# Optimization experiments

Measured on AMD Instinct MI355X. Metric: run time of the kernel, lower is better.

## Reference

```python
import jax, jax.numpy as jnp
import numpy as np

V, E, T_MAX, H, L = 20000, 384, 512, 8, 8
D = E // H  # head size 48
FF = 4 * E


def setup_inputs() -> dict:
    key = jax.random.key(0)
    ks = jax.random.split(key, 24)
    B, T = 16, 512
    s = 0.02
    return {
        "index": jax.random.randint(ks[0], (B, T), 0, V, dtype=jnp.int64),
        "targets": jax.random.randint(ks[1], (B, T), 0, V, dtype=jnp.int64),
        "tok_emb": s * jax.random.normal(ks[2], (V, E), jnp.float32),
        "pos_emb": s * jax.random.normal(ks[3], (T_MAX, E), jnp.float32),
        "Wq": s * jax.random.normal(ks[4], (L, E, H, D), jnp.float32),
        "bq": jnp.zeros((L, H, D), jnp.float32),
        "Wk": s * jax.random.normal(ks[5], (L, E, H, D), jnp.float32),
        "bk": jnp.zeros((L, H, D), jnp.float32),
        "Wv": s * jax.random.normal(ks[6], (L, E, H, D), jnp.float32),
        "bv": jnp.zeros((L, H, D), jnp.float32),
        "Wo": s * jax.random.normal(ks[7], (L, E, E), jnp.float32),
        "bo": jnp.zeros((L, E), jnp.float32),
        "ln1_g": jnp.ones((L, E), jnp.float32),
        "ln1_b": jnp.zeros((L, E), jnp.float32),
        "ln2_g": jnp.ones((L, E), jnp.float32),
        "ln2_b": jnp.zeros((L, E), jnp.float32),
        "W1": s * jax.random.normal(ks[8], (L, E, FF), jnp.float32),
        "b1": jnp.zeros((L, FF), jnp.float32),
        "W2": s * jax.random.normal(ks[9], (L, FF, E), jnp.float32),
        "b2": jnp.zeros((L, E), jnp.float32),
        "lnf_g": jnp.ones((E,), jnp.float32),
        "lnf_b": jnp.zeros((E,), jnp.float32),
        "lm_b": jnp.zeros((V,), jnp.float32),
    }


def layernorm(x, g, b, eps=1e-5):
    mu = jnp.mean(x, axis=-1, keepdims=True)
    var = jnp.var(x, axis=-1, keepdims=True)
    return (x - mu) * jax.lax.rsqrt(var + eps) * g + b


def reference(index, targets, tok_emb, pos_emb, Wq, bq, Wk, bk, Wv, bv, Wo, bo,
              ln1_g, ln1_b, ln2_g, ln2_b, W1, b1, W2, b2, lnf_g, lnf_b, lm_b):
    B, T = index.shape
    x = tok_emb[index] + pos_emb[:T]  # [B,T,E]
    causal = jnp.tril(jnp.ones((T, T), bool))
    scale = D ** -0.5
    for l in range(L):
        h = layernorm(x, ln1_g[l], ln1_b[l])
        q = jnp.einsum('bte,ehd->bthd', h, Wq[l]) + bq[l]
        k = jnp.einsum('bte,ehd->bthd', h, Wk[l]) + bk[l]
        v = jnp.einsum('bte,ehd->bthd', h, Wv[l]) + bv[l]
        scores = jnp.einsum('bqhd,bkhd->bhqk', q, k) * scale
        scores = jnp.where(causal, scores, -jnp.inf)
        w = jax.nn.softmax(scores, axis=-1)
        attn = jnp.einsum('bhqk,bkhd->bqhd', w, v).reshape(B, T, E)
        x = x + attn @ Wo[l] + bo[l]
        h2 = layernorm(x, ln2_g[l], ln2_b[l])
        ff = jax.nn.gelu(h2 @ W1[l] + b1[l], approximate=False) @ W2[l] + b2[l]
        x = x + ff
    x = layernorm(x, lnf_g, lnf_b)
    logits = x @ tok_emb.T + lm_b  # tied weights
    logits = logits.reshape(B * T, V)
    logp = jax.nn.log_softmax(logits, axis=-1)
    loss = -jnp.mean(jnp.take_along_axis(logp, targets.reshape(-1, 1), axis=-1))
    return logits, loss
```

## Files before the change

kernel.cpp:

```cpp
#include <hip/hip_runtime.h>
#include <hip/hip_bf16.h>
#include <math.h>

#define M_ROWS 8192
#define E_DIM 384
#define FF_DIM 1536
#define V_DIM 20000
#define VPAD 20096
#define N_LAYER 8
#define QK_SCALE 0.14433756729740643f
#define PSTRIDE 320
#define NPART 314

typedef __bf16 bf16x8 __attribute__((ext_vector_type(8)));
typedef short  s16x8  __attribute__((ext_vector_type(8)));
typedef float  f32x4  __attribute__((ext_vector_type(4)));
typedef __hip_bfloat16 bf16_t;

__device__ __forceinline__ void gl2lds16(const void* g, void* l) {
    __builtin_amdgcn_global_load_lds((const __attribute__((address_space(1))) void*)g,
                                     (__attribute__((address_space(3))) void*)l, 16, 0, 0);
}
__device__ __forceinline__ unsigned short bf16bits(float v) {
    return __builtin_bit_cast(unsigned short, __float2bfloat16(v));
}

__global__ __launch_bounds__(256) void tconv_kernel(
    const float* __restrict__ in, bf16_t* __restrict__ out,
    int K, int N, int outRows, int rowoff)
{
    __shared__ float tile[32][33];
    const int n0 = blockIdx.x * 32, k0 = blockIdx.y * 32;
    const float* ip = in + (size_t)blockIdx.z * K * N;
    bf16_t* op = out + (size_t)blockIdx.z * outRows * K;
    const int tx = threadIdx.x & 31, ty = threadIdx.x >> 5;
#pragma unroll
    for (int i = 0; i < 32; i += 8)
        tile[ty + i][tx] = ip[(size_t)(k0 + ty + i) * N + n0 + tx];
    __syncthreads();
#pragma unroll
    for (int i = 0; i < 32; i += 8)
        op[(size_t)(rowoff + n0 + ty + i) * K + k0 + tx] = __float2bfloat16(tile[tx][ty + i]);
}

__global__ __launch_bounds__(256) void tokconv_kernel(
    const float* __restrict__ tok, bf16_t* __restrict__ out)
{
    const size_t total = (size_t)VPAD * E_DIM;
    for (size_t i = blockIdx.x * 256ull + threadIdx.x; i < total; i += gridDim.x * 256ull) {
        int row = (int)(i / E_DIM);
        int col = (int)(i - (size_t)row * E_DIM);
        float v = (row < V_DIM) ? tok[(size_t)row * E_DIM + col] : 0.f;
        out[i] = __float2bfloat16(v);
    }
}

__global__ __launch_bounds__(256) void bqkv_kernel(
    const float* __restrict__ bq, const float* __restrict__ bk,
    const float* __restrict__ bv, float* __restrict__ o)
{
    int i = blockIdx.x * 256 + threadIdx.x;
    if (i < N_LAYER * 1152) {
        int l = i / 1152, c = i - l * 1152;
        float v = (c < 384) ? bq[l * 384 + c] : (c < 768) ? bk[l * 384 + c - 384] : bv[l * 384 + c - 768];
        o[i] = v;
    }
}

__global__ __launch_bounds__(256) void embed_kernel(
    const int* __restrict__ idx, const float* __restrict__ tok,
    const float* __restrict__ pos, float* __restrict__ x)
{
    int row = blockIdx.x * 4 + (threadIdx.x >> 6);
    int lane = threadIdx.x & 63;
    int t = row & 511;
    int id = idx[row];
    const float* tr = tok + (size_t)id * E_DIM;
    const float* pr = pos + (size_t)t * E_DIM;
    float* xr = x + (size_t)row * E_DIM;
#pragma unroll
    for (int i = 0; i < 6; i++) { int c = lane + i * 64; xr[c] = tr[c] + pr[c]; }
}

__global__ __launch_bounds__(256) void ln_kernel(
    const float* __restrict__ x, const float* __restrict__ g,
    const float* __restrict__ b, bf16_t* __restrict__ out)
{
    int row = blockIdx.x * 4 + (threadIdx.x >> 6);
    int lane = threadIdx.x & 63;
    const float* xr = x + (size_t)row * E_DIM;
    float vals[6];
    float s = 0.f;
#pragma unroll
    for (int i = 0; i < 6; i++) { vals[i] = xr[lane + i * 64]; s += vals[i]; }
#pragma unroll
    for (int off = 1; off < 64; off <<= 1) s += __shfl_xor(s, off);
    float mu = s * (1.f / E_DIM);
    float sq = 0.f;
#pragma unroll
    for (int i = 0; i < 6; i++) { float d = vals[i] - mu; sq += d * d; }
#pragma unroll
    for (int off = 1; off < 64; off <<= 1) sq += __shfl_xor(sq, off);
    float rstd = rsqrtf(sq * (1.f / E_DIM) + 1e-5f);
    bf16_t* orow = out + (size_t)row * E_DIM;
#pragma unroll
    for (int i = 0; i < 6; i++) {
        int c = lane + i * 64;
        orow[c] = __float2bfloat16((vals[i] - mu) * rstd * g[c] + b[c]);
    }
}

template <int MODE, int MREP, bool SWAP>
__global__ __launch_bounds__(256) void gemm_kernel(
    const bf16_t* __restrict__ A, const bf16_t* __restrict__ Bt,
    const float* __restrict__ bias, void* __restrict__ Cv, void* __restrict__ C2,
    int Ncols, int K)
{
    constexpr int BMR = MREP * 32;
    constexpr int BUFSH = BMR * 32 + 4096;
    __shared__ __align__(16) short smem[2 * BUFSH];
    const int t = threadIdx.x;
    const int w = t >> 6, lane = t & 63;
    const int wm = w >> 1, wn = w & 1;
    const int bm = (MODE == 3 ? blockIdx.x : blockIdx.y) * BMR;
    const int bn = (MODE == 3 ? blockIdx.y : blockIdx.x) * 128;

    f32x4 acc[MREP][4];
#pragma unroll
    for (int m = 0; m < MREP; m++)
#pragma unroll
        for (int n = 0; n < 4; n++)
            acc[m][n] = (f32x4){0.f, 0.f, 0.f, 0.f};

    const int lg = lane >> 4;
    const int ll = lane & 15;
    const int nt = K / 32;

    auto stagef = [&](int kt, int buf) {
        short* sA = smem + buf * BUFSH;
        short* sB = sA + BMR * 32;
#pragma unroll
        for (int i = 0; i < MREP / 2; i++) {
            int li = i * 256 + t;
            int g = li >> (MREP == 4 ? 7 : 6);
            int row = li & (BMR - 1);
            gl2lds16(A + (size_t)(bm + row) * K + kt + g * 8,
                     sA + (size_t)(i * 256 + w * 64) * 8);
        }
#pragma unroll
        for (int i = 0; i < 2; i++) {
            int li = i * 256 + t;
            gl2lds16(Bt + (size_t)(bn + (li & 127)) * K + kt + (li >> 7) * 8,
                     sB + (size_t)(i * 256 + w * 64) * 8);
        }
    };

    stagef(0, 0);
    asm volatile("s_waitcnt vmcnt(0)" ::: "memory");
    __builtin_amdgcn_s_barrier();

    for (int tt = 0; tt < nt; ++tt) {
        const int cur = tt & 1;
        if (tt + 1 < nt) stagef((tt + 1) * 32, cur ^ 1);

        const short* sA = smem + cur * BUFSH;
        const short* sB = sA + BMR * 32;
        bf16x8 af[MREP], bfr[4];
#pragma unroll
        for (int m = 0; m < MREP; m++)
            af[m] = __builtin_bit_cast(bf16x8,
                *(const s16x8*)&sA[(lg * BMR + wm * (BMR / 2) + m * 16 + ll) * 8]);
#pragma unroll
        for (int n = 0; n < 4; n++)
            bfr[n] = __builtin_bit_cast(bf16x8,
                *(const s16x8*)&sB[(lg * 128 + wn * 64 + n * 16 + ll) * 8]);
#pragma unroll
        for (int m = 0; m < MREP; m++)
#pragma unroll
            for (int n = 0; n < 4; n++) {
                if (SWAP)
                    acc[m][n] = __builtin_amdgcn_mfma_f32_16x16x32_bf16(bfr[n], af[m], acc[m][n], 0, 0, 0);
                else
                    acc[m][n] = __builtin_amdgcn_mfma_f32_16x16x32_bf16(af[m], bfr[n], acc[m][n], 0, 0, 0);
            }

        asm volatile("s_waitcnt vmcnt(0)" ::: "memory");
        __builtin_amdgcn_s_barrier();
    }

    if constexpr (SWAP) {
        const int rowm0 = bm + wm * (BMR / 2) + ll;
        const int coln0 = bn + wn * 64 + lg * 4;

        if constexpr (MODE == 4) {
            bf16_t* qkvb = (bf16_t*)Cv;
            const float sc = (bn >= 384) ? 1.f : QK_SCALE;
#pragma unroll
            for (int n = 0; n < 4; n++) {
                const int coln = coln0 + n * 16;
                const float4 b4 = *(const float4*)&bias[coln];
#pragma unroll
                for (int m = 0; m < MREP; m++) {
                    const int row = rowm0 + m * 16;
                    ushort4 pk;
                    pk.x = bf16bits((acc[m][n][0] + b4.x) * sc);
                    pk.y = bf16bits((acc[m][n][1] + b4.y) * sc);
                    pk.z = bf16bits((acc[m][n][2] + b4.z) * sc);
                    pk.w = bf16bits((acc[m][n][3] + b4.w) * sc);
                    *(ushort4*)&qkvb[(size_t)row * 1152 + coln] = pk;
                }
            }
        } else if constexpr (MODE == 1) {
            float* C = (float*)Cv;
#pragma unroll
            for (int n = 0; n < 4; n++) {
                const int coln = coln0 + n * 16;
                const float4 b4 = *(const float4*)&bias[coln];
#pragma unroll
                for (int m = 0; m < MREP; m++) {
                    const int row = rowm0 + m * 16;
                    float4 cv = *(float4*)&C[(size_t)row * Ncols + coln];
                    cv.x += acc[m][n][0] + b4.x;
                    cv.y += acc[m][n][1] + b4.y;
                    cv.z += acc[m][n][2] + b4.z;
                    cv.w += acc[m][n][3] + b4.w;
                    *(float4*)&C[(size_t)row * Ncols + coln] = cv;
                }
            }
        } else if constexpr (MODE == 2) {
            bf16_t* O = (bf16_t*)Cv;
#pragma unroll
            for (int n = 0; n < 4; n++) {
                const int coln = coln0 + n * 16;
                const float4 b4 = *(const float4*)&bias[coln];
#pragma unroll
                for (int m = 0; m < MREP; m++) {
                    const int row = rowm0 + m * 16;
                    float v0 = acc[m][n][0] + b4.x, v1 = acc[m][n][1] + b4.y;
                    float v2 = acc[m][n][2] + b4.z, v3 = acc[m][n][3] + b4.w;
                    v0 = 0.5f * v0 * (1.f + erff(v0 * 0.70710678118654752f));
                    v1 = 0.5f * v1 * (1.f + erff(v1 * 0.70710678118654752f));
                    v2 = 0.5f * v2 * (1.f + erff(v2 * 0.70710678118654752f));
                    v3 = 0.5f * v3 * (1.f + erff(v3 * 0.70710678118654752f));
                    ushort4 pk;
                    pk.x = bf16bits(v0); pk.y = bf16bits(v1);
                    pk.z = bf16bits(v2); pk.w = bf16bits(v3);
                    *(ushort4*)&O[(size_t)row * Ncols + coln] = pk;
                }
            }
        } else if constexpr (MODE == 3) {
            float* C = (float*)Cv;
            float* pbuf = (float*)C2;
            const int ptile = blockIdx.y * 2 + wn;
#pragma unroll
            for (int m = 0; m < MREP; m++) {
                const int row = rowm0 + m * 16;
                float se = 0.f;
#pragma unroll
                for (int n = 0; n < 4; n++) {
                    const int coln = coln0 + n * 16;
                    if (coln + 3 < Ncols) {
                        const float4 b4 = *(const float4*)&bias[coln];
                        float4 v;
                        v.x = acc[m][n][0] + b4.x;
                        v.y = acc[m][n][1] + b4.y;
                        v.z = acc[m][n][2] + b4.z;
                        v.w = acc[m][n][3] + b4.w;
                        *(float4*)&C[(size_t)row * Ncols + coln] = v;
                        se += __expf(v.x) + __expf(v.y) + __expf(v.z) + __expf(v.w);
                    } else {
#pragma unroll
                        for (int e = 0; e < 4; e++) {
                            int col = coln + e;
                            if (col < Ncols) {
                                float v = acc[m][n][e] + bias[col];
                                C[(size_t)row * Ncols + col] = v;
                                se += __expf(v);
                            }
                        }
                    }
                }
                se += __shfl_xor(se, 16);
                se += __shfl_xor(se, 32);
                if (lg == 0) pbuf[(size_t)row * PSTRIDE + ptile] = se;
            }
        }
        return;
    }

    {
        const int r0 = bm + wm * (BMR / 2) + lg * 4;
        const int c0 = bn + wn * 64 + ll;
        bf16_t* vtb = (bf16_t*)C2;
#pragma unroll
        for (int n = 0; n < 4; n++) {
            const int col = c0 + n * 16;
            const float bv = bias[col];
            const int hh = col / 48, dd = col - hh * 48;
#pragma unroll
            for (int m = 0; m < MREP; m++) {
                const int row0 = r0 + m * 16;
                const int bb = row0 >> 9, tt2 = row0 & 511;
                ushort4 pk;
                pk.x = bf16bits(acc[m][n][0] + bv);
                pk.y = bf16bits(acc[m][n][1] + bv);
                pk.z = bf16bits(acc[m][n][2] + bv);
                pk.w = bf16bits(acc[m][n][3] + bv);
                *(ushort4*)&vtb[((size_t)(bb * 8 + hh) * 48 + dd) * 512 + tt2] = pk;
            }
        }
    }
}

__global__ __launch_bounds__(256) void attn_kernel(
    const bf16_t* __restrict__ qkvb, const bf16_t* __restrict__ vt,
    bf16_t* __restrict__ o)
{
    const int qt = blockIdx.x, bh = blockIdx.y;
    const int b = bh >> 3, h = bh & 7;
    __shared__ unsigned short psm[4608];
    const int tid = threadIdx.x;
    const int w = tid >> 6, lane = tid & 63;
    const int ll = lane & 15, g = lane >> 4;
    const int q0 = qt * 64;
    const int q_abs = q0 + ll * 4 + w;

    const bf16_t* qrow = qkvb + (size_t)(b * 512 + q_abs) * 1152 + h * 48;
    bf16x8 qf0 = __builtin_bit_cast(bf16x8, *(const s16x8*)(qrow + g * 8));
    bf16x8 qf1 = {};
    if (g < 2) qf1 = __builtin_bit_cast(bf16x8, *(const s16x8*)(qrow + 32 + g * 8));

    f32x4 oacc[3];
#pragma unroll
    for (int df = 0; df < 3; df++) oacc[df] = (f32x4){0.f, 0.f, 0.f, 0.f};
    float mrun = -1e30f, ssum = 0.f;

    const bf16_t* kptr = qkvb + (size_t)b * 512 * 1152 + 384 + h * 48;
    const bf16_t* vptr = vt + (size_t)bh * 48 * 512;
    const int ntiles = 2 * (qt + 1);

    auto loadK = [&](int kbase, bf16x8& c00, bf16x8& c01, bf16x8& c10, bf16x8& c11) {
        const bf16_t* kr0 = kptr + (size_t)(kbase + ll) * 1152;
        const bf16_t* kr1 = kptr + (size_t)(kbase + 16 + ll) * 1152;
        c00 = __builtin_bit_cast(bf16x8, *(const s16x8*)(kr0 + g * 8));
        c10 = __builtin_bit_cast(bf16x8, *(const s16x8*)(kr1 + g * 8));
        bf16x8 z = {};
        c01 = (g < 2) ? __builtin_bit_cast(bf16x8, *(const s16x8*)(kr0 + 32 + g * 8)) : z;
        c11 = (g < 2) ? __builtin_bit_cast(bf16x8, *(const s16x8*)(kr1 + 32 + g * 8)) : z;
    };

    auto doTile = [&](int kbase, int parity,
                      const bf16x8& c00, const bf16x8& c01, const bf16x8& c10, const bf16x8& c11,
                      bool pf, int nbase,
                      bf16x8& n00, bf16x8& n01, bf16x8& n10, bf16x8& n11) {
        bf16x8 vf[3];
#pragma unroll
        for (int df = 0; df < 3; df++)
            vf[df] = __builtin_bit_cast(bf16x8,
                *(const s16x8*)(vptr + (size_t)(df * 16 + ll) * 512 + kbase + g * 8));
        if (pf) loadK(nbase, n00, n01, n10, n11);

        f32x4 sfr[2];
        {
            f32x4 z0 = {0.f, 0.f, 0.f, 0.f};
            z0 = __builtin_amdgcn_mfma_f32_16x16x32_bf16(c00, qf0, z0, 0, 0, 0);
            z0 = __builtin_amdgcn_mfma_f32_16x16x32_bf16(c01, qf1, z0, 0, 0, 0);
            sfr[0] = z0;
            f32x4 z1 = {0.f, 0.f, 0.f, 0.f};
            z1 = __builtin_amdgcn_mfma_f32_16x16x32_bf16(c10, qf0, z1, 0, 0, 0);
            z1 = __builtin_amdgcn_mfma_f32_16x16x32_bf16(c11, qf1, z1, 0, 0, 0);
            sfr[1] = z1;
        }

        float p[8];
        float tmax = -1e30f;
#pragma unroll
        for (int f = 0; f < 2; f++)
#pragma unroll
            for (int j = 0; j < 4; j++) {
                int key = kbase + f * 16 + g * 4 + j;
                float sv = sfr[f][j];
                sv = (key > q_abs) ? -1e30f : sv;
                p[f * 4 + j] = sv;
                tmax = fmaxf(tmax, sv);
            }
        tmax = fmaxf(tmax, __shfl_xor(tmax, 16));
        tmax = fmaxf(tmax, __shfl_xor(tmax, 32));
        float mnew = fmaxf(mrun, tmax);
        float corr = __expf(mrun - mnew);
        float psum = 0.f;
#pragma unroll
        for (int i = 0; i < 8; i++) { p[i] = __expf(p[i] - mnew); psum += p[i]; }
        psum += __shfl_xor(psum, 16);
        psum += __shfl_xor(psum, 32);
        ssum = ssum * corr + psum;
        mrun = mnew;
#pragma unroll
        for (int df = 0; df < 3; df++)
#pragma unroll
            for (int j = 0; j < 4; j++) oacc[df][j] *= corr;

        const int pbase = (w * 2 + parity) * 576;
#pragma unroll
        for (int f = 0; f < 2; f++)
#pragma unroll
            for (int j = 0; j < 4; j++)
                psm[pbase + (f * 16 + g * 4 + j) * 18 + ll] = bf16bits(p[f * 4 + j]);
        s16x8 pr;
#pragma unroll
        for (int i = 0; i < 8; i++)
            pr[i] = (short)psm[pbase + (g * 8 + i) * 18 + ll];
        bf16x8 pfr = __builtin_bit_cast(bf16x8, pr);
#pragma unroll
        for (int df = 0; df < 3; df++)
            oacc[df] = __builtin_amdgcn_mfma_f32_16x16x32_bf16(vf[df], pfr, oacc[df], 0, 0, 0);
    };

    bf16x8 kA0, kA1, kA2, kA3, kB0, kB1, kB2, kB3;
    loadK(0, kA0, kA1, kA2, kA3);
    for (int kt = 0; kt < ntiles; kt += 2) {
        doTile(kt * 32, 0, kA0, kA1, kA2, kA3,
               true, (kt + 1) * 32, kB0, kB1, kB2, kB3);
        doTile((kt + 1) * 32, 1, kB0, kB1, kB2, kB3,
               (kt + 2) < ntiles, (kt + 2) * 32, kA0, kA1, kA2, kA3);
    }

    float inv = 1.f / ssum;
    bf16_t* orow = o + (size_t)(b * 512 + q_abs) * 384 + h * 48;
#pragma unroll
    for (int df = 0; df < 3; df++) {
        ushort4 pk;
        pk.x = bf16bits(oacc[df][0] * inv);
        pk.y = bf16bits(oacc[df][1] * inv);
        pk.z = bf16bits(oacc[df][2] * inv);
        pk.w = bf16bits(oacc[df][3] * inv);
        *(ushort4*)&orow[df * 16 + g * 4] = pk;
    }
}

__global__ __launch_bounds__(256) void loss_row2_kernel(
    const float* __restrict__ pbuf, const float* __restrict__ logits,
    const int* __restrict__ targets, float* __restrict__ rowloss)
{
    int row = blockIdx.x * 4 + (threadIdx.x >> 6);
    int lane = threadIdx.x & 63;
    const float* pr = pbuf + (size_t)row * PSTRIDE;
    float s = 0.f;
    for (int i = lane; i < NPART; i += 64) s += pr[i];
#pragma unroll
    for (int off = 1; off < 64; off <<= 1) s += __shfl_xor(s, off);
    if (lane == 0) {
        int tgt = targets[row];
        rowloss[row] = logf(s) - logits[(size_t)row * V_DIM + tgt];
    }
}

__global__ __launch_bounds__(256) void loss_reduce_kernel(
    const float* __restrict__ rowloss, float* __restrict__ out)
{
    int t = threadIdx.x;
    __shared__ float red[4];
    float s = 0.f;
    for (int i = t; i < M_ROWS; i += 256) s += rowloss[i];
#pragma unroll
    for (int off = 1; off < 64; off <<= 1) s += __shfl_xor(s, off);
    if ((t & 63) == 0) red[t >> 6] = s;
    __syncthreads();
    if (t == 0) out[0] = (red[0] + red[1] + red[2] + red[3]) * (1.f / M_ROWS);
}

extern "C" void kernel_launch(void* const* d_in, const int* in_sizes, int n_in,
                              void* d_out, int out_size, void* d_ws, size_t ws_size,
                              hipStream_t stream)
{
    const int*   index   = (const int*)d_in[0];
    const int*   targets = (const int*)d_in[1];
    const float* tok_emb = (const float*)d_in[2];
    const float* pos_emb = (const float*)d_in[3];
    const float* Wq = (const float*)d_in[4];
    const float* bq = (const float*)d_in[5];
    const float* Wk = (const float*)d_in[6];
    const float* bk = (const float*)d_in[7];
    const float* Wv = (const float*)d_in[8];
    const float* bv = (const float*)d_in[9];
    const float* Wo = (const float*)d_in[10];
    const float* bo = (const float*)d_in[11];
    const float* ln1_g = (const float*)d_in[12];
    const float* ln1_b = (const float*)d_in[13];
    const float* ln2_g = (const float*)d_in[14];
    const float* ln2_b = (const float*)d_in[15];
    const float* W1 = (const float*)d_in[16];
    const float* b1 = (const float*)d_in[17];
    const float* W2 = (const float*)d_in[18];
    const float* b2 = (const float*)d_in[19];
    const float* lnf_g = (const float*)d_in[20];
    const float* lnf_b = (const float*)d_in[21];
    const float* lm_b  = (const float*)d_in[22];

    float* out = (float*)d_out;
    char* wsb = (char*)d_ws;

    float*  x     = (float*)(wsb + 0);
    bf16_t* hbuf  = (bf16_t*)(wsb + 12582912);
    bf16_t* obuf  = (bf16_t*)(wsb + 18874368);
    bf16_t* qkvb  = (bf16_t*)(wsb + 25165824);
    bf16_t* vtb   = (bf16_t*)(wsb + 44040192);
    bf16_t* ffmid = (bf16_t*)(wsb + 18874368);
    float*  pbuf  = (float*)(wsb + 25165824);
    bf16_t* tokb  = (bf16_t*)(wsb + 50331648);
    bf16_t* qkvw  = (bf16_t*)(wsb + 65765376);
    bf16_t* wo_t  = (bf16_t*)(wsb + 72843264);
    bf16_t* w1_t  = (bf16_t*)(wsb + 75202560);
    bf16_t* w2_t  = (bf16_t*)(wsb + 84639744);
    float*  bqkv  = (float*)(wsb + 94076928);
    float*  rowloss = (float*)(wsb + 94113792);

    tokconv_kernel<<<2048, 256, 0, stream>>>(tok_emb, tokb);
    tconv_kernel<<<dim3(12, 12, 8), 256, 0, stream>>>(Wq, qkvw, 384, 384, 1152, 0);
    tconv_kernel<<<dim3(12, 12, 8), 256, 0, stream>>>(Wk, qkvw, 384, 384, 1152, 384);
    tconv_kernel<<<dim3(12, 12, 8), 256, 0, stream>>>(Wv, qkvw, 384, 384, 1152, 768);
    tconv_kernel<<<dim3(12, 12, 8), 256, 0, stream>>>(Wo, wo_t, 384, 384, 384, 0);
    tconv_kernel<<<dim3(48, 12, 8), 256, 0, stream>>>(W1, w1_t, 384, 1536, 1536, 0);
    tconv_kernel<<<dim3(12, 48, 8), 256, 0, stream>>>(W2, w2_t, 1536, 384, 384, 0);
    bqkv_kernel<<<36, 256, 0, stream>>>(bq, bk, bv, bqkv);

    embed_kernel<<<2048, 256, 0, stream>>>(index, tok_emb, pos_emb, x);

    for (int l = 0; l < N_LAYER; l++) {
        const bf16_t* qkvw_l = qkvw + (size_t)l * 1152 * 384;
        const float*  bqkv_l = bqkv + l * 1152;
        ln_kernel<<<2048, 256, 0, stream>>>(x, ln1_g + l * E_DIM, ln1_b + l * E_DIM, hbuf);
        gemm_kernel<4, 4, true><<<dim3(6, 64), 256, 0, stream>>>(
            hbuf, qkvw_l, bqkv_l, qkvb, nullptr, 1152, 384);
        gemm_kernel<5, 4, false><<<dim3(3, 64), 256, 0, stream>>>(
            hbuf, qkvw_l + (size_t)768 * 384, bqkv_l + 768, nullptr, vtb, 384, 384);
        attn_kernel<<<dim3(8, 128), 256, 0, stream>>>(qkvb, vtb, obuf);
        gemm_kernel<1, 2, true><<<dim3(3, 128), 256, 0, stream>>>(
            obuf, wo_t + (size_t)l * 384 * 384, bo + l * E_DIM, x, nullptr, 384, 384);
        ln_kernel<<<2048, 256, 0, stream>>>(x, ln2_g + l * E_DIM, ln2_b + l * E_DIM, hbuf);
        gemm_kernel<2, 4, true><<<dim3(12, 64), 256, 0, stream>>>(
            hbuf, w1_t + (size_t)l * 1536 * 384, b1 + l * FF_DIM, ffmid, nullptr, 1536, 384);
        gemm_kernel<1, 2, true><<<dim3(3, 128), 256, 0, stream>>>(
            ffmid, w2_t + (size_t)l * 384 * 1536, b2 + l * E_DIM, x, nullptr, 384, 1536);
    }

    ln_kernel<<<2048, 256, 0, stream>>>(x, lnf_g, lnf_b, hbuf);
    gemm_kernel<3, 4, true><<<dim3(64, 157), 256, 0, stream>>>(
        hbuf, tokb, lm_b, out, pbuf, V_DIM, 384);

    loss_row2_kernel<<<2048, 256, 0, stream>>>(pbuf, out, targets, rowloss);
    loss_reduce_kernel<<<1, 256, 0, stream>>>(rowloss, out + (size_t)M_ROWS * V_DIM);
}
```

Baseline: 1.968 ms.

## Triple-buffer GEMM staging, fuse V projection into QKV GEMM, nontemporal logits stores

The GEMM main loop moves from double to triple buffering. Loads are issued two K-tiles ahead, with partial vmcnt waits taken before the barrier instead of draining all loads after the MFMAs. The separate V-transposed GEMM launch is folded into the QKV GEMM: blocks whose columns fall in the V range write a transposed layout with scalar strided stores, and the attention kernel's V pointer is adjusted to match. The LM-head logits and partial sums are written with nontemporal stores to limit cache pollution. In exchange, the kernel needs more LDS, which may lower occupancy, and the scalar transposed V stores are uncoalesced.

```diff
diff --git a/kernel.cpp b/kernel.cpp
--- a/kernel.cpp
+++ b/kernel.cpp
@@ -110,15 +110,17 @@
     }
 }
 
-template <int MODE, int MREP, bool SWAP>
+template <int MODE, int MREP>
 __global__ __launch_bounds__(256) void gemm_kernel(
     const bf16_t* __restrict__ A, const bf16_t* __restrict__ Bt,
     const float* __restrict__ bias, void* __restrict__ Cv, void* __restrict__ C2,
     int Ncols, int K)
 {
     constexpr int BMR = MREP * 32;
-    constexpr int BUFSH = BMR * 32 + 4096;
-    __shared__ __align__(16) short smem[2 * BUFSH];
+    constexpr int ASH = BMR * 32;
+    constexpr int BUFSH = ASH + 4096;
+    constexpr int NLD = MREP / 2 + 2;
+    __shared__ __align__(16) short smem[3 * BUFSH];
     const int t = threadIdx.x;
     const int w = t >> 6, lane = t & 63;
     const int wm = w >> 1, wn = w & 1;
@@ -138,7 +140,7 @@
 
     auto stagef = [&](int kt, int buf) {
         short* sA = smem + buf * BUFSH;
-        short* sB = sA + BMR * 32;
+        short* sB = sA + ASH;
 #pragma unroll
         for (int i = 0; i < MREP / 2; i++) {
             int li = i * 256 + t;
@@ -156,15 +158,21 @@
     };
 
     stagef(0, 0);
-    asm volatile("s_waitcnt vmcnt(0)" ::: "memory");
-    __builtin_amdgcn_s_barrier();
+    stagef(32, 1);
 
     for (int tt = 0; tt < nt; ++tt) {
-        const int cur = tt & 1;
-        if (tt + 1 < nt) stagef((tt + 1) * 32, cur ^ 1);
-
-        const short* sA = smem + cur * BUFSH;
-        const short* sB = sA + BMR * 32;
+        if (tt + 2 < nt) {
+            stagef((tt + 2) * 32, (tt + 2) % 3);
+            asm volatile("s_waitcnt vmcnt(%0)" :: "n"(2 * NLD) : "memory");
+        } else if (tt + 1 < nt) {
+            asm volatile("s_waitcnt vmcnt(%0)" :: "n"(NLD) : "memory");
+        } else {
+            asm volatile("s_waitcnt vmcnt(0)" ::: "memory");
+        }
+        __builtin_amdgcn_s_barrier();
+
+        const short* sA = smem + (tt % 3) * BUFSH;
+        const short* sB = sA + ASH;
         bf16x8 af[MREP], bfr[4];
 #pragma unroll
         for (int m = 0; m < MREP; m++)
@@ -177,22 +185,17 @@
 #pragma unroll
         for (int m = 0; m < MREP; m++)
 #pragma unroll
-            for (int n = 0; n < 4; n++) {
-                if (SWAP)
-                    acc[m][n] = __builtin_amdgcn_mfma_f32_16x16x32_bf16(bfr[n], af[m], acc[m][n], 0, 0, 0);
-                else
-                    acc[m][n] = __builtin_amdgcn_mfma_f32_16x16x32_bf16(af[m], bfr[n], acc[m][n], 0, 0, 0);
-            }
-
-        asm volatile("s_waitcnt vmcnt(0)" ::: "memory");
+            for (int n = 0; n < 4; n++)
+                acc[m][n] = __builtin_amdgcn_mfma_f32_16x16x32_bf16(bfr[n], af[m], acc[m][n], 0, 0, 0);
+
         __builtin_amdgcn_s_barrier();
     }
 
-    if constexpr (SWAP) {
-        const int rowm0 = bm + wm * (BMR / 2) + ll;
-        const int coln0 = bn + wn * 64 + lg * 4;
-
-        if constexpr (MODE == 4) {
+    const int rowm0 = bm + wm * (BMR / 2) + ll;
+    const int coln0 = bn + wn * 64 + lg * 4;
+
+    if constexpr (MODE == 4) {
+        if (bn < 768) {
             bf16_t* qkvb = (bf16_t*)Cv;
             const float sc = (bn >= 384) ? 1.f : QK_SCALE;
 #pragma unroll
@@ -210,104 +213,98 @@
                     *(ushort4*)&qkvb[(size_t)row * 1152 + coln] = pk;
                 }
             }
-        } else if constexpr (MODE == 1) {
-            float* C = (float*)Cv;
+        } else {
+            bf16_t* vtb = (bf16_t*)C2;
+            const int cc0 = coln0 - 768;
+#pragma unroll
+            for (int n = 0; n < 4; n++) {
+                const float4 b4 = *(const float4*)&bias[coln0 + n * 16];
+#pragma unroll
+                for (int m = 0; m < MREP; m++) {
+                    const int row = rowm0 + m * 16;
+                    const int bb = row >> 9, tt2 = row & 511;
+                    bf16_t* vb = vtb + (size_t)bb * 384 * 512 + tt2;
+                    vb[(size_t)(cc0 + n * 16 + 0) * 512] = __float2bfloat16(acc[m][n][0] + b4.x);
+                    vb[(size_t)(cc0 + n * 16 + 1) * 512] = __float2bfloat16(acc[m][n][1] + b4.y);
+                    vb[(size_t)(cc0 + n * 16 + 2) * 512] = __float2bfloat16(acc[m][n][2] + b4.z);
+                    vb[(size_t)(cc0 + n * 16 + 3) * 512] = __float2bfloat16(acc[m][n][3] + b4.w);
+                }
+            }
+        }
+    } else if constexpr (MODE == 1) {
+        float* C = (float*)Cv;
+#pragma unroll
+        for (int n = 0; n < 4; n++) {
+            const int coln = coln0 + n * 16;
+            const float4 b4 = *(const float4*)&bias[coln];
+#pragma unroll
+            for (int m = 0; m < MREP; m++) {
+                const int row = rowm0 + m * 16;
+                float4 cv = *(float4*)&C[(size_t)row * Ncols + coln];
+                cv.x += acc[m][n][0] + b4.x;
+                cv.y += acc[m][n][1] + b4.y;
+                cv.z += acc[m][n][2] + b4.z;
+                cv.w += acc[m][n][3] + b4.w;
+                *(float4*)&C[(size_t)row * Ncols + coln] = cv;
+            }
+        }
+    } else if constexpr (MODE == 2) {
+        bf16_t* O = (bf16_t*)Cv;
+#pragma unroll
+        for (int n = 0; n < 4; n++) {
+            const int coln = coln0 + n * 16;
+            const float4 b4 = *(const float4*)&bias[coln];
+#pragma unroll
+            for (int m = 0; m < MREP; m++) {
+                const int row = rowm0 + m * 16;
+                float v0 = acc[m][n][0] + b4.x, v1 = acc[m][n][1] + b4.y;
+                float v2 = acc[m][n][2] + b4.z, v3 = acc[m][n][3] + b4.w;
+                v0 = 0.5f * v0 * (1.f + erff(v0 * 0.70710678118654752f));
+                v1 = 0.5f * v1 * (1.f + erff(v1 * 0.70710678118654752f));
+                v2 = 0.5f * v2 * (1.f + erff(v2 * 0.70710678118654752f));
+                v3 = 0.5f * v3 * (1.f + erff(v3 * 0.70710678118654752f));
+                ushort4 pk;
+                pk.x = bf16bits(v0); pk.y = bf16bits(v1);
+                pk.z = bf16bits(v2); pk.w = bf16bits(v3);
+                *(ushort4*)&O[(size_t)row * Ncols + coln] = pk;
+            }
+        }
+    } else if constexpr (MODE == 3) {
+        float* C = (float*)Cv;
+        float* pbuf = (float*)C2;
+        const int ptile = blockIdx.y * 2 + wn;
+#pragma unroll
+        for (int m = 0; m < MREP; m++) {
+            const int row = rowm0 + m * 16;
+            float se = 0.f;
 #pragma unroll
             for (int n = 0; n < 4; n++) {
                 const int coln = coln0 + n * 16;
-                const float4 b4 = *(const float4*)&bias[coln];
-#pragma unroll
-                for (int m = 0; m < MREP; m++) {
-                    const int row = rowm0 + m * 16;
-                    float4 cv = *(float4*)&C[(size_t)row * Ncols + coln];
-                    cv.x += acc[m][n][0] + b4.x;
-                    cv.y += acc[m][n][1] + b4.y;
-                    cv.z += acc[m][n][2] + b4.z;
-                    cv.w += acc[m][n][3] + b4.w;
-                    *(float4*)&C[(size_t)row * Ncols + coln] = cv;
-                }
-            }
-        } else if constexpr (MODE == 2) {
-            bf16_t* O = (bf16_t*)Cv;
-#pragma unroll
-            for (int n = 0; n < 4; n++) {
-                const int coln = coln0 + n * 16;
-                const float4 b4 = *(const float4*)&bias[coln];
-#pragma unroll
-                for (int m = 0; m < MREP; m++) {
-                    const int row = rowm0 + m * 16;
-                    float v0 = acc[m][n][0] + b4.x, v1 = acc[m][n][1] + b4.y;
-                    float v2 = acc[m][n][2] + b4.z, v3 = acc[m][n][3] + b4.w;
-                    v0 = 0.5f * v0 * (1.f + erff(v0 * 0.70710678118654752f));
-                    v1 = 0.5f * v1 * (1.f + erff(v1 * 0.70710678118654752f));
-                    v2 = 0.5f * v2 * (1.f + erff(v2 * 0.70710678118654752f));
-                    v3 = 0.5f * v3 * (1.f + erff(v3 * 0.70710678118654752f));
-                    ushort4 pk;
-                    pk.x = bf16bits(v0); pk.y = bf16bits(v1);
-                    pk.z = bf16bits(v2); pk.w = bf16bits(v3);
-                    *(ushort4*)&O[(size_t)row * Ncols + coln] = pk;
-                }
-            }
-        } else if constexpr (MODE == 3) {
-            float* C = (float*)Cv;
-            float* pbuf = (float*)C2;
-            const int ptile = blockIdx.y * 2 + wn;
-#pragma unroll
-            for (int m = 0; m < MREP; m++) {
-                const int row = rowm0 + m * 16;
-                float se = 0.f;
-#pragma unroll
-                for (int n = 0; n < 4; n++) {
-                    const int coln = coln0 + n * 16;
-                    if (coln + 3 < Ncols) {
-                        const float4 b4 = *(const float4*)&bias[coln];
-                        float4 v;
-                        v.x = acc[m][n][0] + b4.x;
-                        v.y = acc[m][n][1] + b4.y;
-                        v.z = acc[m][n][2] + b4.z;
-                        v.w = acc[m][n][3] + b4.w;
-                        *(float4*)&C[(size_t)row * Ncols + coln] = v;
-                        se += __expf(v.x) + __expf(v.y) + __expf(v.z) + __expf(v.w);
-                    } else {
-#pragma unroll
-                        for (int e = 0; e < 4; e++) {
-                            int col = coln + e;
-                            if (col < Ncols) {
-                                float v = acc[m][n][e] + bias[col];
-                                C[(size_t)row * Ncols + col] = v;
-                                se += __expf(v);
-                            }
+                if (coln + 3 < Ncols) {
+                    const float4 b4 = *(const float4*)&bias[coln];
+                    f32x4 v;
+                    v[0] = acc[m][n][0] + b4.x;
+                    v[1] = acc[m][n][1] + b4.y;
+                    v[2] = acc[m][n][2] + b4.z;
+                    v[3] = acc[m][n][3] + b4.w;
+                    __builtin_nontemporal_store(v, (f32x4*)&C[(size_t)row * Ncols + coln]);
+                    se += __expf(v[0]) + __expf(v[1]) + __expf(v[2]) + __expf(v[3]);
+                } else {
+#pragma unroll
+                    for (int e = 0; e < 4; e++) {
+                        int col = coln + e;
+                        if (col < Ncols) {
+                            float v = acc[m][n][e] + bias[col];
+                            __builtin_nontemporal_store(v, &C[(size_t)row * Ncols + col]);
+                            se += __expf(v);
                         }
                     }
                 }
-                se += __shfl_xor(se, 16);
-                se += __shfl_xor(se, 32);
-                if (lg == 0) pbuf[(size_t)row * PSTRIDE + ptile] = se;
             }
-        }
-        return;
-    }
-
-    {
-        const int r0 = bm + wm * (BMR / 2) + lg * 4;
-        const int c0 = bn + wn * 64 + ll;
-        bf16_t* vtb = (bf16_t*)C2;
-#pragma unroll
-        for (int n = 0; n < 4; n++) {
-            const int col = c0 + n * 16;
-            const float bv = bias[col];
-            const int hh = col / 48, dd = col - hh * 48;
-#pragma unroll
-            for (int m = 0; m < MREP; m++) {
-                const int row0 = r0 + m * 16;
-                const int bb = row0 >> 9, tt2 = row0 & 511;
-                ushort4 pk;
-                pk.x = bf16bits(acc[m][n][0] + bv);
-                pk.y = bf16bits(acc[m][n][1] + bv);
-                pk.z = bf16bits(acc[m][n][2] + bv);
-                pk.w = bf16bits(acc[m][n][3] + bv);
-                *(ushort4*)&vtb[((size_t)(bb * 8 + hh) * 48 + dd) * 512 + tt2] = pk;
-            }
+            se += __shfl_xor(se, 16);
+            se += __shfl_xor(se, 32);
+            if (lg == 0)
+                __builtin_nontemporal_store(se, &pbuf[(size_t)row * PSTRIDE + ptile]);
         }
     }
 }
@@ -336,7 +333,7 @@
     float mrun = -1e30f, ssum = 0.f;
 
     const bf16_t* kptr = qkvb + (size_t)b * 512 * 1152 + 384 + h * 48;
-    const bf16_t* vptr = vt + (size_t)bh * 48 * 512;
+    const bf16_t* vptr = vt + (size_t)(bh >> 3) * 384 * 512 + (size_t)(bh & 7) * 48 * 512;
     const int ntiles = 2 * (qt + 1);
 
     auto loadK = [&](int kbase, bf16x8& c00, bf16x8& c01, bf16x8& c10, bf16x8& c11) {
@@ -530,22 +527,20 @@
         const bf16_t* qkvw_l = qkvw + (size_t)l * 1152 * 384;
         const float*  bqkv_l = bqkv + l * 1152;
         ln_kernel<<<2048, 256, 0, stream>>>(x, ln1_g + l * E_DIM, ln1_b + l * E_DIM, hbuf);
-        gemm_kernel<4, 4, true><<<dim3(6, 64), 256, 0, stream>>>(
-            hbuf, qkvw_l, bqkv_l, qkvb, nullptr, 1152, 384);
-        gemm_kernel<5, 4, false><<<dim3(3, 64), 256, 0, stream>>>(
-            hbuf, qkvw_l + (size_t)768 * 384, bqkv_l + 768, nullptr, vtb, 384, 384);
+        gemm_kernel<4, 4><<<dim3(9, 64), 256, 0, stream>>>(
+            hbuf, qkvw_l, bqkv_l, qkvb, vtb, 1152, 384);
         attn_kernel<<<dim3(8, 128), 256, 0, stream>>>(qkvb, vtb, obuf);
-        gemm_kernel<1, 2, true><<<dim3(3, 128), 256, 0, stream>>>(
+        gemm_kernel<1, 2><<<dim3(3, 128), 256, 0, stream>>>(
             obuf, wo_t + (size_t)l * 384 * 384, bo + l * E_DIM, x, nullptr, 384, 384);
         ln_kernel<<<2048, 256, 0, stream>>>(x, ln2_g + l * E_DIM, ln2_b + l * E_DIM, hbuf);
-        gemm_kernel<2, 4, true><<<dim3(12, 64), 256, 0, stream>>>(
+        gemm_kernel<2, 4><<<dim3(12, 64), 256, 0, stream>>>(
             hbuf, w1_t + (size_t)l * 1536 * 384, b1 + l * FF_DIM, ffmid, nullptr, 1536, 384);
-        gemm_kernel<1, 2, true><<<dim3(3, 128), 256, 0, stream>>>(
+        gemm_kernel<1, 2><<<dim3(3, 128), 256, 0, stream>>>(
             ffmid, w2_t + (size_t)l * 384 * 1536, b2 + l * E_DIM, x, nullptr, 384, 1536);
     }
 
     ln_kernel<<<2048, 256, 0, stream>>>(x, lnf_g, lnf_b, hbuf);
-    gemm_kernel<3, 4, true><<<dim3(64, 157), 256, 0, stream>>>(
+    gemm_kernel<3, 4><<<dim3(64, 157), 256, 0, stream>>>(
         hbuf, tokb, lm_b, out, pbuf, V_DIM, 384);
 
     loss_row2_kernel<<<2048, 256, 0, stream>>>(pbuf, out, targets, rowloss);
```

Result: faster. 1.836 ms (-6.7%).
